# Kernel optimization log

Measured on AMD Instinct MI355X. Metric: run time of the kernel, lower is better.

Reference implementation:

```python
import jax, jax.numpy as jnp
import numpy as np

KERNEL = 3
STRIDE = 1
PADDING = 1


def _extract_patches(x, k, stride, padding, h_out, w_out):
    # x: [B, C, H, W] -> patches [k, k, B, C, h_out, w_out]
    if padding > 0:
        x = jnp.pad(x, ((0, 0), (0, 0), (padding, padding), (padding, padding)))
    rows = []
    for di in range(k):
        cols = []
        for dj in range(k):
            sl = x[:, :, di:di + (h_out - 1) * stride + 1:stride,
                        dj:dj + (w_out - 1) * stride + 1:stride]
            cols.append(sl)
        rows.append(jnp.stack(cols, axis=0))
    return jnp.stack(rows, axis=0)  # [k, k, B, C, h_out, w_out]


def setup_inputs() -> dict:
    key = jax.random.key(0)
    k1, k2 = jax.random.split(key)
    B, C_in, C_out, H, W = 32, 64, 64, 32, 32
    h_out = (H + 2 * PADDING - KERNEL) // STRIDE + 1
    w_out = (W + 2 * PADDING - KERNEL) // STRIDE + 1
    fan_in = C_in * KERNEL ** 2
    x = jax.random.normal(k1, (B, C_in, H, W), dtype=jnp.float32)
    weight = jax.random.normal(
        k2, (h_out, w_out, C_out, C_in, KERNEL, KERNEL), dtype=jnp.float32
    ) / np.sqrt(fan_in).astype(np.float32)
    bias = jnp.zeros((C_out, h_out, w_out), dtype=jnp.float32)
    return {"x": x, "weight": weight, "bias": bias}


def reference(x, weight, bias):
    h_out, w_out = weight.shape[0], weight.shape[1]
    # patches: [k, k, B, C, h_out, w_out]
    patches = _extract_patches(x, KERNEL, STRIDE, PADDING, h_out, w_out)
    # unshared-weight contraction per spatial location
    # weight: [h_out(x), w_out(y), O, C(i), k(k), k(l)]
    out = jnp.einsum('xyoikl,klbixy->boxy', weight, patches)
    return out + bias[None, :, :, :]
```

## Files before the change

### kernel.cpp

```cpp
#include <hip/hip_runtime.h>

#define HH 32
#define WW 32
#define CIN 64
#define COUT 64
#define BATCH 32
#define KTOT 576
#define NPOS 1024
#define KC 8
#define KHALF 288
#define NCW 36
#define WGRP 260

__device__ float g_xT[CIN * 34 * 34 * BATCH];

__global__ __launch_bounds__(256) void repack_kernel(const float* __restrict__ x) {
    __shared__ float tile[32 * 33];
    const int i   = blockIdx.x;
    const int hh  = blockIdx.y;
    const int tid = threadIdx.x;

    float* dst = &g_xT[((i * 34 + hh) * 34) * BATCH];

    if (hh == 0 || hh == 33) {
        for (int idx = tid; idx < 34 * BATCH; idx += 256) dst[idx] = 0.f;
        return;
    }
    const int hs = hh - 1;
#pragma unroll
    for (int bb = 0; bb < 4; ++bb) {
        int b = bb * 8 + (tid >> 5);
        int w = tid & 31;
        tile[b * 33 + w] = x[(b << 16) + (i << 10) + (hs << 5) + w];
    }
    __syncthreads();
#pragma unroll
    for (int q = 0; q < 5; ++q) {
        int ww = q * 8 + (tid >> 5);
        if (ww < 34) {
            int b = tid & 31;
            float v = (ww == 0 || ww == 33) ? 0.f : tile[b * 33 + (ww - 1)];
            dst[ww * BATCH + b] = v;
        }
    }
}

__device__ __forceinline__ void async16(const void* src, void* dst_lds) {
    __builtin_amdgcn_global_load_lds(
        (const __attribute__((address_space(1))) void*)src,
        (__attribute__((address_space(3))) void*)dst_lds,
        16, 0, 0);
}

__global__ __launch_bounds__(128, 2) void local2d_kernel(
    const float* __restrict__ weight,
    const float* __restrict__ bias,
    float* __restrict__ out)
{
    __shared__ float Wl[2][3][2 * WGRP];
    __shared__ float Pl[2][3][KC * BATCH];

    const int wv = threadIdx.x >> 6;
    const int l  = threadIdx.x & 63;

    const int og = l & 7, bg = l >> 3;

    int bid = blockIdx.x;
    int xcd = bid & 7;
    int t   = bid >> 3;
    int y   = ((t >> 5) << 3) | xcd;
    int xw  = t & 31;
    int p   = (y << 5) | xw;

    const int kbase = wv * KHALF;
    const float* wpos  = weight + (long)p * (COUT * KTOT);
    const float* wsrc0 = wpos + (l >> 1) * KTOT + ((l & 1) << 2) + kbase;

    float acc[8][4];
#pragma unroll
    for (int a = 0; a < 8; ++a)
#pragma unroll
        for (int c = 0; c < 4; ++c) acc[a][c] = 0.f;

    auto stage = [&](int c, int bsel) {
        const float* ws = wsrc0 + c * KC;
#pragma unroll
        for (int g = 0; g < 2; ++g)
            async16(ws + g * (32 * KTOT), &Wl[wv][bsel][g * WGRP]);
        {
            int k  = kbase + c * KC + (l >> 3);
            int i  = k / 9;
            int r  = k - i * 9;
            int kh = r / 3;
            int kw = r - kh * 3;
            const float* ps =
                &g_xT[(((i * 34) + y + kh) * 34 + xw + kw) * BATCH + ((l & 7) << 2)];
            async16(ps, &Pl[wv][bsel][0]);
        }
    };

    auto compute = [&](int bsel) {
        const float* Wb = &Wl[wv][bsel][(og >> 2) * WGRP + ((og & 3) << 3) * KC];
        const float* Pb = &Pl[wv][bsel][bg << 2];
#pragma unroll
        for (int kk = 0; kk < KC; kk += 4) {
            float4 pr[4];
#pragma unroll
            for (int j = 0; j < 4; ++j)
                pr[j] = *(const float4*)(Pb + (kk + j) * BATCH);
            const float* prf = (const float*)pr;
#pragma unroll
            for (int oo = 0; oo < 8; ++oo) {
                float4 wr = *(const float4*)(Wb + oo * KC + kk);
#pragma unroll
                for (int bb = 0; bb < 4; ++bb) {
                    float a = acc[oo][bb];
                    a = fmaf(wr.x, prf[0 * 4 + bb], a);
                    a = fmaf(wr.y, prf[1 * 4 + bb], a);
                    a = fmaf(wr.z, prf[2 * 4 + bb], a);
                    a = fmaf(wr.w, prf[3 * 4 + bb], a);
                    acc[oo][bb] = a;
                }
            }
        }
    };

    stage(0, 0);
    stage(1, 1);
    for (int c = 0; c < NCW - 1; ++c) {
        asm volatile("s_waitcnt vmcnt(3)" ::: "memory");
        asm volatile("s_waitcnt lgkmcnt(0)" ::: "memory");
        if (c + 2 < NCW) stage(c + 2, (c + 2) % 3);
        compute(c % 3);
    }
    asm volatile("s_waitcnt vmcnt(0)" ::: "memory");
    compute((NCW - 1) % 3);

    __syncthreads();
    float* R = &Wl[0][0][0];
    if (wv == 1) {
#pragma unroll
        for (int oo = 0; oo < 8; ++oo) {
            int o = (og << 3) + oo;
            *(float4*)(&R[o * 36 + (bg << 2)]) =
                make_float4(acc[oo][0], acc[oo][1], acc[oo][2], acc[oo][3]);
        }
    }
    __syncthreads();
    if (wv == 0) {
#pragma unroll
        for (int oo = 0; oo < 8; ++oo) {
            int o = (og << 3) + oo;
            float bv = bias[(o << 10) + p];
            float4 r = *(const float4*)(&R[o * 36 + (bg << 2)]);
            const float* rf = (const float*)&r;
#pragma unroll
            for (int bb = 0; bb < 4; ++bb) {
                int b = (bg << 2) + bb;
                out[(b << 16) + (o << 10) + p] = acc[oo][bb] + rf[bb] + bv;
            }
        }
    }
}

extern "C" void kernel_launch(void* const* d_in, const int* in_sizes, int n_in,
                              void* d_out, int out_size, void* d_ws, size_t ws_size,
                              hipStream_t stream) {
    const float* x      = (const float*)d_in[0];
    const float* weight = (const float*)d_in[1];
    const float* bias   = (const float*)d_in[2];
    float* out          = (float*)d_out;

    hipLaunchKernelGGL(repack_kernel, dim3(CIN, 34), dim3(256), 0, stream, x);
    hipLaunchKernelGGL(local2d_kernel, dim3(NPOS), dim3(128), 0, stream,
                       weight, bias, out);
}
```

Baseline: 258.5 us.

## Split output channels across two blocks per position to double grid size

Each block now computes half of the output channels (32) for one spatial position, doubling the grid to 2048 blocks and halving per-thread accumulators and weight staging. The weight LDS layout is reorganised so one 16-byte async load per lane fills the tile, and the wait count is adjusted to match. This is meant to raise occupancy and parallelism for a memory-bound weight stream. In exchange, the patch data is loaded twice (once per half) and the per-block overhead is doubled.

```diff
diff --git a/kernel.cpp b/kernel.cpp
--- a/kernel.cpp
+++ b/kernel.cpp
@@ -10,7 +10,6 @@
 #define KC 8
 #define KHALF 288
 #define NCW 36
-#define WGRP 260
 
 __device__ float g_xT[CIN * 34 * 34 * BATCH];
 
@@ -57,7 +56,7 @@
     const float* __restrict__ bias,
     float* __restrict__ out)
 {
-    __shared__ float Wl[2][3][2 * WGRP];
+    __shared__ float Wl[2][3][32 * KC];
     __shared__ float Pl[2][3][KC * BATCH];
 
     const int wv = threadIdx.x >> 6;
@@ -68,25 +67,25 @@
     int bid = blockIdx.x;
     int xcd = bid & 7;
     int t   = bid >> 3;
-    int y   = ((t >> 5) << 3) | xcd;
-    int xw  = t & 31;
+    int oh  = t & 1;
+    int tt  = t >> 1;
+    int y   = ((tt >> 5) << 3) | xcd;
+    int xw  = tt & 31;
     int p   = (y << 5) | xw;
 
     const int kbase = wv * KHALF;
-    const float* wpos  = weight + (long)p * (COUT * KTOT);
-    const float* wsrc0 = wpos + (l >> 1) * KTOT + ((l & 1) << 2) + kbase;
+    const float* wpos = weight + ((long)p * COUT + (oh << 5)) * KTOT;
+    const float* wsrc0 =
+        wpos + (((l & 7) << 2) + (l >> 4)) * KTOT + (((l >> 3) & 1) << 2) + kbase;
 
-    float acc[8][4];
+    float acc[4][4];
 #pragma unroll
-    for (int a = 0; a < 8; ++a)
+    for (int a = 0; a < 4; ++a)
 #pragma unroll
         for (int c = 0; c < 4; ++c) acc[a][c] = 0.f;
 
     auto stage = [&](int c, int bsel) {
-        const float* ws = wsrc0 + c * KC;
-#pragma unroll
-        for (int g = 0; g < 2; ++g)
-            async16(ws + g * (32 * KTOT), &Wl[wv][bsel][g * WGRP]);
+        async16(wsrc0 + c * KC, &Wl[wv][bsel][0]);
         {
             int k  = kbase + c * KC + (l >> 3);
             int i  = k / 9;
@@ -100,7 +99,7 @@
     };
 
     auto compute = [&](int bsel) {
-        const float* Wb = &Wl[wv][bsel][(og >> 2) * WGRP + ((og & 3) << 3) * KC];
+        const float* Wb = &Wl[wv][bsel][og << 2];
         const float* Pb = &Pl[wv][bsel][bg << 2];
 #pragma unroll
         for (int kk = 0; kk < KC; kk += 4) {
@@ -110,8 +109,8 @@
                 pr[j] = *(const float4*)(Pb + (kk + j) * BATCH);
             const float* prf = (const float*)pr;
 #pragma unroll
-            for (int oo = 0; oo < 8; ++oo) {
-                float4 wr = *(const float4*)(Wb + oo * KC + kk);
+            for (int oo = 0; oo < 4; ++oo) {
+                float4 wr = *(const float4*)(Wb + (oo << 6) + (kk << 3));
 #pragma unroll
                 for (int bb = 0; bb < 4; ++bb) {
                     float a = acc[oo][bb];
@@ -128,7 +127,7 @@
     stage(0, 0);
     stage(1, 1);
     for (int c = 0; c < NCW - 1; ++c) {
-        asm volatile("s_waitcnt vmcnt(3)" ::: "memory");
+        asm volatile("s_waitcnt vmcnt(2)" ::: "memory");
         asm volatile("s_waitcnt lgkmcnt(0)" ::: "memory");
         if (c + 2 < NCW) stage(c + 2, (c + 2) % 3);
         compute(c % 3);
@@ -140,8 +139,8 @@
     float* R = &Wl[0][0][0];
     if (wv == 1) {
 #pragma unroll
-        for (int oo = 0; oo < 8; ++oo) {
-            int o = (og << 3) + oo;
+        for (int oo = 0; oo < 4; ++oo) {
+            int o = (og << 2) + oo;
             *(float4*)(&R[o * 36 + (bg << 2)]) =
                 make_float4(acc[oo][0], acc[oo][1], acc[oo][2], acc[oo][3]);
         }
@@ -149,15 +148,16 @@
     __syncthreads();
     if (wv == 0) {
 #pragma unroll
-        for (int oo = 0; oo < 8; ++oo) {
-            int o = (og << 3) + oo;
-            float bv = bias[(o << 10) + p];
+        for (int oo = 0; oo < 4; ++oo) {
+            int o  = (og << 2) + oo;
+            int of = (oh << 5) + o;
+            float bv = bias[(of << 10) + p];
             float4 r = *(const float4*)(&R[o * 36 + (bg << 2)]);
             const float* rf = (const float*)&r;
 #pragma unroll
             for (int bb = 0; bb < 4; ++bb) {
                 int b = (bg << 2) + bb;
-                out[(b << 16) + (o << 10) + p] = acc[oo][bb] + rf[bb] + bv;
+                out[(b << 16) + (of << 10) + p] = acc[oo][bb] + rf[bb] + bv;
             }
         }
     }
@@ -172,6 +172,6 @@
     float* out          = (float*)d_out;
 
     hipLaunchKernelGGL(repack_kernel, dim3(CIN, 34), dim3(256), 0, stream, x);
-    hipLaunchKernelGGL(local2d_kernel, dim3(NPOS), dim3(128), 0, stream,
+    hipLaunchKernelGGL(local2d_kernel, dim3(2 * NPOS), dim3(128), 0, stream,
                        weight, bias, out);
 }
```

After: 252.9 us. 2.2% less time.
